# Kernel tuning notes

Hardware: AMD Instinct MI355X
Metric: run time of the kernel (lower is better)

## Reference

```python
import jax, jax.numpy as jnp
import numpy as np


def setup_inputs() -> dict:
    key = jax.random.key(0)
    ks = jax.random.split(key, 9)
    B, T, S, D = 4, 256, 256, 512
    scale = 1.0 / np.sqrt(D)
    inp = {
        "output": jax.random.normal(ks[0], (B, T, D), dtype=jnp.float32),
        "context": jax.random.normal(ks[1], (B, S, D), dtype=jnp.float32),
        "mask": jax.random.randint(ks[2], (B, S), 0, 2, dtype=jnp.int32),
        # learned params (nn.Linear stores y = x @ W.T + b; we store W.T directly)
        "Wq": jax.random.normal(ks[3], (D, D), dtype=jnp.float32) * scale,
        "bq": jax.random.normal(ks[4], (D,), dtype=jnp.float32) * scale,
        "Wc": jax.random.normal(ks[5], (D, D), dtype=jnp.float32) * scale,
        "v": jax.random.normal(ks[6], (D,), dtype=jnp.float32) * scale,
        "Wout": jax.random.normal(ks[7], (2 * D, D), dtype=jnp.float32) * scale,
        "bout": jax.random.normal(ks[8], (D,), dtype=jnp.float32) * scale,
    }
    return inp


def reference(output, context, mask, Wq, bq, Wc, v, Wout, bout):
    # output: (B, T, D) decoder states; context: (B, S, D) encoder states
    wq = jnp.einsum("btd,de->bte", output, Wq) + bq          # (B, T, D)
    uh = jnp.einsum("bsd,de->bse", context, Wc)               # (B, S, D)
    # additive score: v . tanh(wq + uh), broadcast over (T, S)
    wquh = jnp.tanh(wq[:, :, None, :] + uh[:, None, :, :])    # (B, T, S, D)
    score = jnp.einsum("btsd,d->bts", wquh, v)                # (B, T, S)
    # masked softmax exactly as the torch code: max over ALL positions,
    # then zero out masked entries (mask==1 means masked) and renormalize.
    max_by_row = jnp.max(score, axis=-1, keepdims=True)
    keep = (1.0 - mask.astype(score.dtype))[:, None, :]       # (B, 1, S)
    attn = jnp.exp(score - max_by_row) * keep
    attn = attn / jnp.sum(attn, axis=-1, keepdims=True)       # (B, T, S)
    mix = jnp.einsum("bts,bsd->btd", attn, context)           # (B, T, D)
    combined = jnp.concatenate([mix, output], axis=-1)        # (B, T, 2D)
    out = jnp.einsum("btf,fd->btd", combined, Wout) + bout    # (B, T, D)
    return out, attn
```

## Files before the change

kernel.cpp:

```cpp
#include <hip/hip_runtime.h>
#include <hip/hip_bf16.h>

#define B_ 4
#define T_ 256
#define S_ 256
#define D_ 512
#define TB 2

typedef __bf16 bf16x8 __attribute__((ext_vector_type(8)));
typedef float  floatx4 __attribute__((ext_vector_type(4)));

#define C2F 2.885390081777926f

static __device__ __forceinline__ unsigned short f2bf(float x) {
    __hip_bfloat16 h = __float2bfloat16(x);
    return *reinterpret_cast<unsigned short*>(&h);
}
static __device__ __forceinline__ float asf(unsigned int u) {
    float f; __builtin_memcpy(&f, &u, 4); return f;
}

struct G3 {
    const float* A;
    const float* W;
    int krow0;
    const float* aux;
    void* C;
    int mode;
};

__global__ __launch_bounds__(256) void gemm3(G3 g0, G3 g1, G3 g2, G3 g3)
{
    const int z = blockIdx.z;
    G3 g = (z == 0) ? g0 : (z == 1) ? g1 : (z == 2) ? g2 : g3;

    const int tid  = threadIdx.x;
    const int wave = tid >> 6, lane = tid & 63;
    const int l15  = lane & 15, quad = lane >> 4;
    const int wm   = wave >> 1, wn = wave & 1;
    const int m0   = blockIdx.y * 64;
    const int n0   = blockIdx.x * 64;

    __shared__ unsigned short Af[4 * 64 * 8];
    __shared__ unsigned short Bf[4 * 64 * 8];

    const int sm  = tid >> 2, skq = tid & 3;
    const int sn  = tid & 63, sk8 = (tid >> 6) * 8;

    const float* Abase = g.A + (size_t)(m0 + sm) * 512 + skq * 8;
    const float* Wbase = g.W + (size_t)(g.krow0 + sk8) * 512 + n0 + sn;

    unsigned short* Awr = Af + ((size_t)(sm >> 4) * 64 + ((sm & 15) | (skq << 4))) * 8;
    unsigned short* Bwr = Bf + ((size_t)(sn >> 4) * 64 + ((sn & 15) | ((sk8 >> 3) << 4))) * 8;

    const unsigned short* Ard0 = Af + ((size_t)(wm * 2 + 0) * 64 + lane) * 8;
    const unsigned short* Ard1 = Af + ((size_t)(wm * 2 + 1) * 64 + lane) * 8;
    const unsigned short* Brd0 = Bf + ((size_t)(wn * 2 + 0) * 64 + lane) * 8;
    const unsigned short* Brd1 = Bf + ((size_t)(wn * 2 + 1) * 64 + lane) * 8;

    floatx4 acc[2][2];
    #pragma unroll
    for (int i = 0; i < 2; ++i)
        #pragma unroll
        for (int j = 0; j < 2; ++j) acc[i][j] = (floatx4){0.f, 0.f, 0.f, 0.f};

    for (int chunk = 0; chunk < 16; ++chunk) {
        const int k0 = chunk * 32;
        float4 a0 = *(const float4*)(Abase + k0);
        float4 a1 = *(const float4*)(Abase + k0 + 4);
        float bcol[8];
        #pragma unroll
        for (int j = 0; j < 8; ++j)
            bcol[j] = Wbase[(size_t)(k0 + j) * 512];

        __syncthreads();
        uint4 pa;
        pa.x = (unsigned)f2bf(a0.x) | ((unsigned)f2bf(a0.y) << 16);
        pa.y = (unsigned)f2bf(a0.z) | ((unsigned)f2bf(a0.w) << 16);
        pa.z = (unsigned)f2bf(a1.x) | ((unsigned)f2bf(a1.y) << 16);
        pa.w = (unsigned)f2bf(a1.z) | ((unsigned)f2bf(a1.w) << 16);
        *(uint4*)Awr = pa;
        uint4 pb;
        pb.x = (unsigned)f2bf(bcol[0]) | ((unsigned)f2bf(bcol[1]) << 16);
        pb.y = (unsigned)f2bf(bcol[2]) | ((unsigned)f2bf(bcol[3]) << 16);
        pb.z = (unsigned)f2bf(bcol[4]) | ((unsigned)f2bf(bcol[5]) << 16);
        pb.w = (unsigned)f2bf(bcol[6]) | ((unsigned)f2bf(bcol[7]) << 16);
        *(uint4*)Bwr = pb;
        __syncthreads();

        bf16x8 fa0 = *(const bf16x8*)Ard0;
        bf16x8 fa1 = *(const bf16x8*)Ard1;
        bf16x8 fb0 = *(const bf16x8*)Brd0;
        bf16x8 fb1 = *(const bf16x8*)Brd1;
        acc[0][0] = __builtin_amdgcn_mfma_f32_16x16x32_bf16(fa0, fb0, acc[0][0], 0, 0, 0);
        acc[0][1] = __builtin_amdgcn_mfma_f32_16x16x32_bf16(fa0, fb1, acc[0][1], 0, 0, 0);
        acc[1][0] = __builtin_amdgcn_mfma_f32_16x16x32_bf16(fa1, fb0, acc[1][0], 0, 0, 0);
        acc[1][1] = __builtin_amdgcn_mfma_f32_16x16x32_bf16(fa1, fb1, acc[1][1], 0, 0, 0);
    }

    #pragma unroll
    for (int mi = 0; mi < 2; ++mi) {
        #pragma unroll
        for (int ni = 0; ni < 2; ++ni) {
            const int col = n0 + wn * 32 + ni * 16 + l15;
            const int rbase = m0 + wm * 32 + mi * 16 + quad * 4;
            if (g.mode == 3) {
                unsigned short* Cb = (unsigned short*)g.C;
                #pragma unroll
                for (int r = 0; r < 4; ++r) {
                    int row = rbase + r, bb = row >> 8, ss = row & 255;
                    Cb[((size_t)(bb * 64 + (col >> 3)) * 256 + ss) * 8 + (col & 7)]
                        = f2bf(C2F * acc[mi][ni][r]);
                }
            } else if (g.mode == 5) {
                unsigned short* Cb = (unsigned short*)g.C;
                #pragma unroll
                for (int r = 0; r < 4; ++r)
                    Cb[(size_t)(rbase + r) * 512 + col] = f2bf(acc[mi][ni][r]);
            } else {
                float* Cf = (float*)g.C;
                float bv = g.aux ? g.aux[col] : 0.0f;
                #pragma unroll
                for (int r = 0; r < 4; ++r) {
                    float val = acc[mi][ni][r] + bv;
                    if (g.mode == 1) val *= C2F;
                    Cf[(size_t)(rbase + r) * 512 + col] = val;
                }
            }
        }
    }
}

__global__ __launch_bounds__(1024) void attn_fused(
    const float* __restrict__ wqs,
    const unsigned short* __restrict__ uhb,
    const unsigned short* __restrict__ CWb,
    const float* __restrict__ OB,
    const int*   __restrict__ mask,
    const float* __restrict__ v,
    float* __restrict__ attn_out,
    float* __restrict__ out)
{
    const int bg  = blockIdx.x;
    const int b   = bg / (T_ / TB);
    const int t0  = (bg % (T_ / TB)) * TB;
    const int tid = threadIdx.x;
    const int s   = tid & 255;
    const int h   = tid >> 8;

    __shared__ float  w_s[TB][D_];
    __shared__ float  v_s[D_];
    __shared__ float2 part[4][256];
    __shared__ float2 wred[4];
    __shared__ float  a_s[TB][256];
    __shared__ float  mixp[4][TB][D_];

    if (tid < 512) {
        w_s[0][tid] = wqs[(size_t)(b * T_ + t0 + 0) * D_ + tid];
        w_s[1][tid] = wqs[(size_t)(b * T_ + t0 + 1) * D_ + tid];
        v_s[tid]    = v[tid];
    }
    __syncthreads();

    float acc0 = 0.f, acc1 = 0.f;
    const int dd0 = h * 16;
    const uint4* u4 = (const uint4*)(uhb + ((size_t)(b * 64 + dd0) * 256 + s) * 8);

    #pragma unroll 4
    for (int dd = 0; dd < 16; ++dd) {
        uint4 uu = u4[(size_t)dd * 256];
        float uf[8];
        uf[0] = asf(uu.x << 16); uf[1] = asf(uu.x & 0xffff0000u);
        uf[2] = asf(uu.y << 16); uf[3] = asf(uu.y & 0xffff0000u);
        uf[4] = asf(uu.z << 16); uf[5] = asf(uu.z & 0xffff0000u);
        uf[6] = asf(uu.w << 16); uf[7] = asf(uu.w & 0xffff0000u);

        const int dbase = (dd0 + dd) * 8;
        #pragma unroll
        for (int j = 0; j < 8; ++j) {
            float vv = v_s[dbase + j];
            float x0 = w_s[0][dbase + j] + uf[j];
            float x1 = w_s[1][dbase + j] + uf[j];
            float r0 = __builtin_amdgcn_rcpf(__builtin_amdgcn_exp2f(x0) + 1.0f);
            float r1 = __builtin_amdgcn_rcpf(__builtin_amdgcn_exp2f(x1) + 1.0f);
            acc0 = fmaf(vv, r0, acc0);
            acc1 = fmaf(vv, r1, acc1);
        }
    }
    part[h][s] = make_float2(acc0, acc1);
    __syncthreads();

    float p0 = 0.f, p1 = 0.f;
    if (tid < 256) {
        float A0 = part[0][tid].x + part[1][tid].x + part[2][tid].x + part[3][tid].x;
        float A1 = part[0][tid].y + part[1][tid].y + part[2][tid].y + part[3][tid].y;
        float keep = 1.0f - (float)mask[b * S_ + tid];
        p0 = __builtin_amdgcn_exp2f(-C2F * A0) * keep;
        p1 = __builtin_amdgcn_exp2f(-C2F * A1) * keep;
        float s0 = p0, s1 = p1;
        #pragma unroll
        for (int off = 1; off < 64; off <<= 1) {
            s0 += __shfl_xor(s0, off);
            s1 += __shfl_xor(s1, off);
        }
        if ((tid & 63) == 0) wred[tid >> 6] = make_float2(s0, s1);
    }
    __syncthreads();

    if (tid < 256) {
        float den0 = wred[0].x + wred[1].x + wred[2].x + wred[3].x;
        float den1 = wred[0].y + wred[1].y + wred[2].y + wred[3].y;
        float a0 = p0 * __builtin_amdgcn_rcpf(den0);
        float a1 = p1 * __builtin_amdgcn_rcpf(den1);
        attn_out[(size_t)(b * T_ + t0 + 0) * S_ + tid] = a0;
        attn_out[(size_t)(b * T_ + t0 + 1) * S_ + tid] = a1;
        a_s[0][tid] = a0;
        a_s[1][tid] = a1;
    }
    __syncthreads();

    const int d2 = tid & 255;
    const int sh = h * 64;
    const unsigned short* cw = CWb + ((size_t)(b * S_) + sh) * D_ + 2 * d2;
    float m[TB][2] = {};
    #pragma unroll 8
    for (int s2 = 0; s2 < 64; ++s2) {
        unsigned int cc = *(const unsigned int*)(cw + (size_t)s2 * D_);
        float c0 = asf(cc << 16), c1 = asf(cc & 0xffff0000u);
        #pragma unroll
        for (int t = 0; t < TB; ++t) {
            float a = a_s[t][sh + s2];
            m[t][0] = fmaf(a, c0, m[t][0]);
            m[t][1] = fmaf(a, c1, m[t][1]);
        }
    }
    #pragma unroll
    for (int t = 0; t < TB; ++t) {
        mixp[h][t][2 * d2]     = m[t][0];
        mixp[h][t][2 * d2 + 1] = m[t][1];
    }
    __syncthreads();

    {
        const int t = tid >> 9, d = tid & 511;
        size_t idx = (size_t)(b * T_ + t0 + t) * D_ + d;
        out[idx] = mixp[0][t][d] + mixp[1][t][d] + mixp[2][t][d] + mixp[3][t][d]
                 + OB[idx];
    }
}

extern "C" void kernel_launch(void* const* d_in, const int* in_sizes, int n_in,
                              void* d_out, int out_size, void* d_ws, size_t ws_size,
                              hipStream_t stream) {
    const float* output  = (const float*)d_in[0];
    const float* context = (const float*)d_in[1];
    const int*   mask    = (const int*)d_in[2];
    const float* Wq      = (const float*)d_in[3];
    const float* bq      = (const float*)d_in[4];
    const float* Wc      = (const float*)d_in[5];
    const float* v       = (const float*)d_in[6];
    const float* Wout    = (const float*)d_in[7];
    const float* bout    = (const float*)d_in[8];

    float* out  = (float*)d_out;
    float* attn = out + (size_t)B_ * T_ * D_;

    char* ws = (char*)d_ws;
    float* wqs          = (float*)ws;
    float* OB           = (float*)(ws + (2u << 20));
    unsigned short* uhb = (unsigned short*)(ws + (4u << 20));
    unsigned short* CWb = (unsigned short*)(ws + (5u << 20));

    G3 gwq = { output,  Wq,     0, bq,      wqs, 1 };
    G3 guh = { context, Wc,     0, nullptr, uhb, 3 };
    G3 gob = { output,  Wout, 512, bout,    OB,  4 };
    G3 gcw = { context, Wout,   0, nullptr, CWb, 5 };
    gemm3<<<dim3(8, 16, 4), dim3(256), 0, stream>>>(gwq, guh, gob, gcw);

    attn_fused<<<dim3(B_ * T_ / TB), dim3(1024), 0, stream>>>(
        wqs, uhb, CWb, OB, mask, v, attn, out);
}
```

Measured before the change: 124.3 us.

## Remap projection GEMM to 1024-thread blocks with one MFMA tile per wave

```diff
diff --git a/kernel.cpp b/kernel.cpp
--- a/kernel.cpp
+++ b/kernel.cpp
@@ -20,7 +20,7 @@
     float f; __builtin_memcpy(&f, &u, 4); return f;
 }
 
-struct G3 {
+struct G4 {
     const float* A;
     const float* W;
     int krow0;
@@ -29,104 +29,80 @@
     int mode;
 };
 
-__global__ __launch_bounds__(256) void gemm3(G3 g0, G3 g1, G3 g2, G3 g3)
+__global__ __launch_bounds__(1024, 8) void gemm4(G4 g0, G4 g1, G4 g2, G4 g3)
 {
-    const int z = blockIdx.z;
-    G3 g = (z == 0) ? g0 : (z == 1) ? g1 : (z == 2) ? g2 : g3;
-
-    const int tid  = threadIdx.x;
-    const int wave = tid >> 6, lane = tid & 63;
-    const int l15  = lane & 15, quad = lane >> 4;
-    const int wm   = wave >> 1, wn = wave & 1;
-    const int m0   = blockIdx.y * 64;
-    const int n0   = blockIdx.x * 64;
+    const int tid = threadIdx.x;
+    const int bid = blockIdx.x;
+
+    const int z  = bid & 3;
+    const int n0 = ((bid >> 2) & 7) * 64;
+    const int m0 = (bid >> 5) * 64;
+
+    G4 g = (z == 0) ? g0 : (z == 1) ? g1 : (z == 2) ? g2 : g3;
 
     __shared__ unsigned short Af[4 * 64 * 8];
     __shared__ unsigned short Bf[4 * 64 * 8];
 
-    const int sm  = tid >> 2, skq = tid & 3;
-    const int sn  = tid & 63, sk8 = (tid >> 6) * 8;
-
-    const float* Abase = g.A + (size_t)(m0 + sm) * 512 + skq * 8;
-    const float* Wbase = g.W + (size_t)(g.krow0 + sk8) * 512 + n0 + sn;
-
-    unsigned short* Awr = Af + ((size_t)(sm >> 4) * 64 + ((sm & 15) | (skq << 4))) * 8;
-    unsigned short* Bwr = Bf + ((size_t)(sn >> 4) * 64 + ((sn & 15) | ((sk8 >> 3) << 4))) * 8;
-
-    const unsigned short* Ard0 = Af + ((size_t)(wm * 2 + 0) * 64 + lane) * 8;
-    const unsigned short* Ard1 = Af + ((size_t)(wm * 2 + 1) * 64 + lane) * 8;
-    const unsigned short* Brd0 = Bf + ((size_t)(wn * 2 + 0) * 64 + lane) * 8;
-    const unsigned short* Brd1 = Bf + ((size_t)(wn * 2 + 1) * 64 + lane) * 8;
-
-    floatx4 acc[2][2];
-    #pragma unroll
-    for (int i = 0; i < 2; ++i)
-        #pragma unroll
-        for (int j = 0; j < 2; ++j) acc[i][j] = (floatx4){0.f, 0.f, 0.f, 0.f};
+    const int am = tid >> 4;
+    const int ak = (tid & 15) * 2;
+    const int bn = tid & 63;
+    const int bk = (tid >> 6) * 2;
+
+    const float* Aptr = g.A + (size_t)(m0 + am) * 512 + ak;
+    const float* Wptr = g.W + (size_t)(g.krow0 + bk) * 512 + n0 + bn;
+
+    unsigned int* Awr = (unsigned int*)&Af[((am >> 4) * 64
+                          + ((am & 15) | ((ak >> 3) << 4))) * 8 + (ak & 7)];
+    unsigned int* Bwr = (unsigned int*)&Bf[((bn >> 4) * 64
+                          + ((bn & 15) | ((bk >> 3) << 4))) * 8 + (bk & 7)];
+
+    const int wave = tid >> 6, lane = tid & 63;
+    const int l15 = lane & 15, quad = lane >> 4;
+    const int mf = wave >> 2, nf = wave & 3;
+    const unsigned short* Ard = &Af[(mf * 64 + lane) * 8];
+    const unsigned short* Brd = &Bf[(nf * 64 + lane) * 8];
+
+    floatx4 acc = (floatx4){0.f, 0.f, 0.f, 0.f};
 
     for (int chunk = 0; chunk < 16; ++chunk) {
         const int k0 = chunk * 32;
-        float4 a0 = *(const float4*)(Abase + k0);
-        float4 a1 = *(const float4*)(Abase + k0 + 4);
-        float bcol[8];
-        #pragma unroll
-        for (int j = 0; j < 8; ++j)
-            bcol[j] = Wbase[(size_t)(k0 + j) * 512];
+        float2 av = *(const float2*)(Aptr + k0);
+        float  b0 = Wptr[(size_t)k0 * 512];
+        float  b1 = Wptr[(size_t)k0 * 512 + 512];
 
         __syncthreads();
-        uint4 pa;
-        pa.x = (unsigned)f2bf(a0.x) | ((unsigned)f2bf(a0.y) << 16);
-        pa.y = (unsigned)f2bf(a0.z) | ((unsigned)f2bf(a0.w) << 16);
-        pa.z = (unsigned)f2bf(a1.x) | ((unsigned)f2bf(a1.y) << 16);
-        pa.w = (unsigned)f2bf(a1.z) | ((unsigned)f2bf(a1.w) << 16);
-        *(uint4*)Awr = pa;
-        uint4 pb;
-        pb.x = (unsigned)f2bf(bcol[0]) | ((unsigned)f2bf(bcol[1]) << 16);
-        pb.y = (unsigned)f2bf(bcol[2]) | ((unsigned)f2bf(bcol[3]) << 16);
-        pb.z = (unsigned)f2bf(bcol[4]) | ((unsigned)f2bf(bcol[5]) << 16);
-        pb.w = (unsigned)f2bf(bcol[6]) | ((unsigned)f2bf(bcol[7]) << 16);
-        *(uint4*)Bwr = pb;
+        *Awr = (unsigned)f2bf(av.x) | ((unsigned)f2bf(av.y) << 16);
+        *Bwr = (unsigned)f2bf(b0)   | ((unsigned)f2bf(b1)   << 16);
         __syncthreads();
 
-        bf16x8 fa0 = *(const bf16x8*)Ard0;
-        bf16x8 fa1 = *(const bf16x8*)Ard1;
-        bf16x8 fb0 = *(const bf16x8*)Brd0;
-        bf16x8 fb1 = *(const bf16x8*)Brd1;
-        acc[0][0] = __builtin_amdgcn_mfma_f32_16x16x32_bf16(fa0, fb0, acc[0][0], 0, 0, 0);
-        acc[0][1] = __builtin_amdgcn_mfma_f32_16x16x32_bf16(fa0, fb1, acc[0][1], 0, 0, 0);
-        acc[1][0] = __builtin_amdgcn_mfma_f32_16x16x32_bf16(fa1, fb0, acc[1][0], 0, 0, 0);
-        acc[1][1] = __builtin_amdgcn_mfma_f32_16x16x32_bf16(fa1, fb1, acc[1][1], 0, 0, 0);
-    }
-
-    #pragma unroll
-    for (int mi = 0; mi < 2; ++mi) {
-        #pragma unroll
-        for (int ni = 0; ni < 2; ++ni) {
-            const int col = n0 + wn * 32 + ni * 16 + l15;
-            const int rbase = m0 + wm * 32 + mi * 16 + quad * 4;
-            if (g.mode == 3) {
-                unsigned short* Cb = (unsigned short*)g.C;
-                #pragma unroll
-                for (int r = 0; r < 4; ++r) {
-                    int row = rbase + r, bb = row >> 8, ss = row & 255;
-                    Cb[((size_t)(bb * 64 + (col >> 3)) * 256 + ss) * 8 + (col & 7)]
-                        = f2bf(C2F * acc[mi][ni][r]);
-                }
-            } else if (g.mode == 5) {
-                unsigned short* Cb = (unsigned short*)g.C;
-                #pragma unroll
-                for (int r = 0; r < 4; ++r)
-                    Cb[(size_t)(rbase + r) * 512 + col] = f2bf(acc[mi][ni][r]);
-            } else {
-                float* Cf = (float*)g.C;
-                float bv = g.aux ? g.aux[col] : 0.0f;
-                #pragma unroll
-                for (int r = 0; r < 4; ++r) {
-                    float val = acc[mi][ni][r] + bv;
-                    if (g.mode == 1) val *= C2F;
-                    Cf[(size_t)(rbase + r) * 512 + col] = val;
-                }
-            }
+        bf16x8 fa = *(const bf16x8*)Ard;
+        bf16x8 fb = *(const bf16x8*)Brd;
+        acc = __builtin_amdgcn_mfma_f32_16x16x32_bf16(fa, fb, acc, 0, 0, 0);
+    }
+
+    const int col = n0 + nf * 16 + l15;
+    const int rbase = m0 + mf * 16 + quad * 4;
+    if (g.mode == 3) {
+        unsigned short* Cb = (unsigned short*)g.C;
+        #pragma unroll
+        for (int r = 0; r < 4; ++r) {
+            int row = rbase + r, bb = row >> 8, ss = row & 255;
+            Cb[((size_t)(bb * 64 + (col >> 3)) * 256 + ss) * 8 + (col & 7)]
+                = f2bf(C2F * acc[r]);
+        }
+    } else if (g.mode == 5) {
+        unsigned short* Cb = (unsigned short*)g.C;
+        #pragma unroll
+        for (int r = 0; r < 4; ++r)
+            Cb[(size_t)(rbase + r) * 512 + col] = f2bf(acc[r]);
+    } else {
+        float* Cf = (float*)g.C;
+        float bv = g.aux ? g.aux[col] : 0.0f;
+        #pragma unroll
+        for (int r = 0; r < 4; ++r) {
+            float val = acc[r] + bv;
+            if (g.mode == 1) val *= C2F;
+            Cf[(size_t)(rbase + r) * 512 + col] = val;
         }
     }
 }
@@ -271,11 +247,11 @@
     unsigned short* uhb = (unsigned short*)(ws + (4u << 20));
     unsigned short* CWb = (unsigned short*)(ws + (5u << 20));
 
-    G3 gwq = { output,  Wq,     0, bq,      wqs, 1 };
-    G3 guh = { context, Wc,     0, nullptr, uhb, 3 };
-    G3 gob = { output,  Wout, 512, bout,    OB,  4 };
-    G3 gcw = { context, Wout,   0, nullptr, CWb, 5 };
-    gemm3<<<dim3(8, 16, 4), dim3(256), 0, stream>>>(gwq, guh, gob, gcw);
+    G4 gwq = { output,  Wq,     0, bq,      wqs, 1 };
+    G4 guh = { context, Wc,     0, nullptr, uhb, 3 };
+    G4 gob = { output,  Wout, 512, bout,    OB,  4 };
+    G4 gcw = { context, Wout,   0, nullptr, CWb, 5 };
+    gemm4<<<dim3(512), dim3(1024), 0, stream>>>(gwq, guh, gob, gcw);
 
     attn_fused<<<dim3(B_ * T_ / TB), dim3(1024), 0, stream>>>(
         wqs, uhb, CWb, OB, mask, v, attn, out);
```

After: 123.7 us. Within noise of the previous version (-0.4%).
